# Performance work log

Hardware: AMD Instinct MI355X
Metric: run time of the kernel (lower is better)

The kernel has to match this reference:

```python
import jax, jax.numpy as jnp
import numpy as np

N = 100000   # nodes
E = 1600000  # edges
G = 64       # graphs in batch
F_IN = 128
H = 128
SV = 64
AD = 32


def setup_inputs() -> dict:
    key = jax.random.key(0)
    ks = jax.random.split(key, 12)
    s = 0.05
    return {
        "x": jax.random.normal(ks[0], (N, F_IN), jnp.float32),
        "edge_index": jax.random.randint(ks[1], (2, E), 0, N, dtype=jnp.int64),
        "batch": jnp.sort(jax.random.randint(ks[2], (N,), 0, G, dtype=jnp.int64)),
        "state_vector": jax.random.normal(ks[3], (G, SV), jnp.float32),
        "action": jax.random.normal(ks[4], (G, AD), jnp.float32),
        "W1": jax.random.normal(ks[5], (F_IN, H), jnp.float32) * s,
        "b1": jnp.zeros((H,), jnp.float32),
        "W2": jax.random.normal(ks[6], (H, H), jnp.float32) * s,
        "b2": jnp.zeros((H,), jnp.float32),
        "Wf1": jax.random.normal(ks[7], (H + SV + AD, 256), jnp.float32) * s,
        "bf1": jnp.zeros((256,), jnp.float32),
        "Wf2": jax.random.normal(ks[8], (256, 256), jnp.float32) * s,
        "bf2": jnp.zeros((256,), jnp.float32),
        "Wo": jax.random.normal(ks[9], (256, 1), jnp.float32) * s,
        "bo": jnp.zeros((1,), jnp.float32),
    }


def gcn_conv(x, W, b, src, dst, deg_inv_sqrt):
    # PyG GCNConv: h = x @ W; aggregate D^-1/2 (A+I) D^-1/2 h; + b
    h = x @ W
    norm = deg_inv_sqrt[src] * deg_inv_sqrt[dst]          # [E]
    agg = jax.ops.segment_sum(h[src] * norm[:, None], dst, num_segments=N)
    agg = agg + h * (deg_inv_sqrt * deg_inv_sqrt)[:, None]  # self loops
    return agg + b


def reference(x, edge_index, batch, state_vector, action,
              W1, b1, W2, b2, Wf1, bf1, Wf2, bf2, Wo, bo):
    src, dst = edge_index[0], edge_index[1]
    # degree after adding self loops (aggregation index = dst, PyG default flow)
    deg = jax.ops.segment_sum(jnp.ones((E,), jnp.float32), dst, num_segments=N) + 1.0
    deg_inv_sqrt = jax.lax.rsqrt(deg)

    h = jax.nn.relu(gcn_conv(x, W1, b1, src, dst, deg_inv_sqrt))
    h = jax.nn.relu(gcn_conv(h, W2, b2, src, dst, deg_inv_sqrt))

    # global_mean_pool over graph ids
    sums = jax.ops.segment_sum(h, batch, num_segments=G)
    cnts = jax.ops.segment_sum(jnp.ones((N,), jnp.float32), batch, num_segments=G)
    pooled = sums / jnp.maximum(cnts, 1.0)[:, None]       # [G, H]

    z = jnp.concatenate([pooled, state_vector, action], axis=1)  # [G, H+SV+AD]
    z = jax.nn.relu(z @ Wf1 + bf1)
    z = jax.nn.relu(z @ Wf2 + bf2)
    return z @ Wo + bo                                     # [G, 1]
```

## Files before the change

### kernel.cpp

```cpp
#include <hip/hip_runtime.h>
#include <hip/hip_bf16.h>
#include <stdint.h>

#define N_NODES 100000
#define N_EDGES 1600000
#define N_GRAPHS 64
#define HDIM 128

#define BUCKET_SHIFT 9
#define NBUCK ((N_NODES + 511) >> 9)
#define CAP 9728
#define SCAT_CHUNK 8192
#define SCAT_NBLK ((N_EDGES + SCAT_CHUNK - 1) / SCAT_CHUNK)
#define GB_NBLK ((N_NODES + 255) / 256)

typedef __bf16 bf16x8 __attribute__((ext_vector_type(8)));
typedef float f32x4 __attribute__((ext_vector_type(4)));
typedef float f32x2 __attribute__((ext_vector_type(2)));

__global__ __launch_bounds__(256) void setup_kernel(const int* __restrict__ batch,
                                                    int* __restrict__ gstart,
                                                    const float* __restrict__ W1,
                                                    const float* __restrict__ W2,
                                                    __hip_bfloat16* __restrict__ Wt1,
                                                    __hip_bfloat16* __restrict__ Wt2,
                                                    int* __restrict__ gcur,
                                                    float* __restrict__ psum) {
    int bid = blockIdx.x;
    if (bid < GB_NBLK) {
        int i = bid * 256 + threadIdx.x;
        if (i >= N_NODES) return;
        int b = batch[i];
        int prev = (i == 0) ? -1 : batch[i - 1];
        for (int g = prev + 1; g <= b; ++g) gstart[g] = i;
        if (i == N_NODES - 1) {
            for (int g = b + 1; g <= N_GRAPHS; ++g) gstart[g] = N_NODES;
        }
    } else if (bid < GB_NBLK + 128) {
        int t = bid - GB_NBLK;
        const float* W = (t < 64) ? W1 : W2;
        __hip_bfloat16* Wt = (t < 64) ? Wt1 : Wt2;
        int bb = t & 63;
        int n = bb * 2 + (threadIdx.x >> 7);
        int k = threadIdx.x & 127;
        Wt[n * 128 + k] = __float2bfloat16(W[k * 128 + n]);
    } else {
        int i = (bid - GB_NBLK - 128) * 256 + threadIdx.x;
        if (i < NBUCK) gcur[i] = i * CAP;
        int j = i - NBUCK;
        if (j >= 0 && j < N_GRAPHS * HDIM) psum[j] = 0.f;
    }
}
#define SETUP_NBLK (GB_NBLK + 128 + (NBUCK + N_GRAPHS * HDIM + 255) / 256)

__global__ __launch_bounds__(256) void scatter_kernel(const int* __restrict__ src,
                                                      const int* __restrict__ dst,
                                                      int* __restrict__ gcur,
                                                      int* __restrict__ sorted, int E) {
    __shared__ int hist[NBUCK];
    __shared__ int base_s[NBUCK];
    int tid = threadIdx.x;
    int e0 = blockIdx.x * SCAT_CHUNK;
    int sv[SCAT_CHUNK / 256], dv[SCAT_CHUNK / 256];
#pragma unroll
    for (int j = 0; j < SCAT_CHUNK / 256; j++) {
        int e = e0 + (j << 8) + tid;
        if (e < E) { sv[j] = src[e]; dv[j] = dst[e]; } else { sv[j] = -1; dv[j] = -1; }
    }
    if (tid < NBUCK) hist[tid] = 0;
    __syncthreads();
#pragma unroll
    for (int j = 0; j < SCAT_CHUNK / 256; j++)
        if (dv[j] >= 0) atomicAdd(&hist[dv[j] >> BUCKET_SHIFT], 1);
    __syncthreads();
    if (tid < NBUCK) {
        int c = hist[tid];
        base_s[tid] = (c > 0) ? atomicAdd(&gcur[tid], c) : 0;
    }
    __syncthreads();
    if (tid < NBUCK) hist[tid] = 0;
    __syncthreads();
#pragma unroll
    for (int j = 0; j < SCAT_CHUNK / 256; j++) {
        if (dv[j] >= 0) {
            int b = dv[j] >> BUCKET_SHIFT;
            int idx = atomicAdd(&hist[b], 1);
            sorted[base_s[b] + idx] = ((dv[j] & 511) << 17) | sv[j];
        }
    }
}

__global__ __launch_bounds__(256) void bucket_build_kernel(const int* __restrict__ sorted,
                                                           const int* __restrict__ gcur,
                                                           int2* __restrict__ rs2,
                                                           float* __restrict__ dis,
                                                           int* __restrict__ csr_src) {
    __shared__ int edges[CAP];
    __shared__ int cnt[512];
    __shared__ int excl[512];
    __shared__ int ps[256];
    int b = blockIdx.x, tid = threadIdx.x;
    cnt[tid] = 0; cnt[tid + 256] = 0;
    int node0 = b << BUCKET_SHIFT;
    int lo = b * CAP, hi = gcur[b];
    int ne = hi - lo;
    for (int i = tid; i < ne; i += 256) edges[i] = sorted[lo + i];
    __syncthreads();
    for (int i = tid; i < ne; i += 256)
        atomicAdd(&cnt[((unsigned)edges[i]) >> 17], 1);
    __syncthreads();
    int c0 = cnt[2 * tid], c1 = cnt[2 * tid + 1];
    ps[tid] = c0 + c1;
    __syncthreads();
#pragma unroll
    for (int off = 1; off < 256; off <<= 1) {
        int t = (tid >= off) ? ps[tid - off] : 0;
        __syncthreads();
        ps[tid] += t;
        __syncthreads();
    }
    int pex = ps[tid] - (c0 + c1);
    excl[2 * tid] = pex;
    excl[2 * tid + 1] = pex + c0;
    __syncthreads();
#pragma unroll
    for (int k = 0; k < 2; k++) {
        int li = tid + k * 256;
        int node = node0 + li;
        if (node < N_NODES) {
            int st = lo + excl[li] + li;
            int c = cnt[li];
            rs2[node] = make_int2(st, st + c + 1);
            dis[node] = rsqrtf((float)c + 1.0f);
            csr_src[st + c] = node;
        }
    }
    cnt[tid] = 0; cnt[tid + 256] = 0;
    __syncthreads();
    for (int i = tid; i < ne; i += 256) {
        int v = edges[i];
        int li = ((unsigned)v) >> 17;
        int idx = atomicAdd(&cnt[li], 1);
        csr_src[lo + excl[li] + li + idx] = v & 0x1FFFF;
    }
}

template<bool A_FP32>
__global__ __launch_bounds__(256) void gemm_mfma_kernel(const void* __restrict__ Av,
                                                        const __hip_bfloat16* __restrict__ Wt,
                                                        const float* __restrict__ scale,
                                                        unsigned char* __restrict__ C, int nrows) {
    __shared__ float Cs[64 * 132];
    int tid = threadIdx.x;
    int wave = tid >> 6, lane = tid & 63;
    int quad = lane >> 4, l16 = lane & 15;
    int row0 = blockIdx.x * 64;
    int arow = row0 + wave * 16 + l16;
    int arow_c = min(arow, nrows - 1);

    const __hip_bfloat16* A16 = (const __hip_bfloat16*)Av;
    const float* A32 = (const float*)Av;

    f32x4 acc[8];
#pragma unroll
    for (int t = 0; t < 8; t++) acc[t] = (f32x4){0.f, 0.f, 0.f, 0.f};

#pragma unroll
    for (int kt = 0; kt < 4; kt++) {
        int kbase = kt * 32 + quad * 8;
        union { bf16x8 v; __hip_bfloat16 h[8]; uint4 u; } au;
        if (A_FP32) {
            const float* ap = A32 + (size_t)arow_c * 128 + kbase;
            float4 u0 = *(const float4*)ap;
            float4 u1 = *(const float4*)(ap + 4);
            au.h[0] = __float2bfloat16(u0.x); au.h[1] = __float2bfloat16(u0.y);
            au.h[2] = __float2bfloat16(u0.z); au.h[3] = __float2bfloat16(u0.w);
            au.h[4] = __float2bfloat16(u1.x); au.h[5] = __float2bfloat16(u1.y);
            au.h[6] = __float2bfloat16(u1.z); au.h[7] = __float2bfloat16(u1.w);
        } else {
            au.u = *(const uint4*)(A16 + (size_t)arow_c * 128 + kbase);
        }
#pragma unroll
        for (int t = 0; t < 8; t++) {
            bf16x8 b = *(const bf16x8*)(Wt + (size_t)(t * 16 + l16) * 128 + kbase);
            acc[t] = __builtin_amdgcn_mfma_f32_16x16x32_bf16(au.v, b, acc[t], 0, 0, 0);
        }
    }

    int rbase = wave * 16 + quad * 4;
    float s[4];
#pragma unroll
    for (int r = 0; r < 4; r++) s[r] = scale[min(row0 + rbase + r, nrows - 1)];
#pragma unroll
    for (int t = 0; t < 8; t++) {
#pragma unroll
        for (int r = 0; r < 4; r++)
            Cs[(rbase + r) * 132 + t * 16 + l16] = acc[t][r] * s[r];
    }
    __syncthreads();

#pragma unroll
    for (int p = 0; p < 4; p++) {
        int g = p * 256 + tid;
        int row = g >> 4, c8 = (g & 15) * 8;
        int grow = row0 + row;
        if (grow < nrows) {
            const float* cp = &Cs[row * 132 + c8];
            float4 v0 = *(const float4*)cp;
            float4 v1 = *(const float4*)(cp + 4);
            int w0 = __builtin_amdgcn_cvt_pk_fp8_f32(v0.x, v0.y, 0, false);
            w0 = __builtin_amdgcn_cvt_pk_fp8_f32(v0.z, v0.w, w0, true);
            int w1 = __builtin_amdgcn_cvt_pk_fp8_f32(v1.x, v1.y, 0, false);
            w1 = __builtin_amdgcn_cvt_pk_fp8_f32(v1.z, v1.w, w1, true);
            *(uint2*)(C + (size_t)grow * 128 + c8) = make_uint2((unsigned)w0, (unsigned)w1);
        }
    }
}

__device__ __forceinline__ void accum8p(f32x2* acc, uint2 u) {
    acc[0] += __builtin_amdgcn_cvt_pk_f32_fp8((int)u.x, false);
    acc[1] += __builtin_amdgcn_cvt_pk_f32_fp8((int)u.x, true);
    acc[2] += __builtin_amdgcn_cvt_pk_f32_fp8((int)u.y, false);
    acc[3] += __builtin_amdgcn_cvt_pk_f32_fp8((int)u.y, true);
}

__global__ __launch_bounds__(256) void agg_kernel(const unsigned char* __restrict__ h8,
                                                  const float* __restrict__ dis,
                                                  const int2* __restrict__ rs2,
                                                  const int* __restrict__ csr_src,
                                                  const float* __restrict__ bias,
                                                  __hip_bfloat16* __restrict__ out, int n) {
    int wid = threadIdx.x >> 6;
    int lane = threadIdx.x & 63;
    int half = lane >> 5;
    int q = lane >> 4;
    int f = lane & 15;
    int l32 = lane & 31;
    int sub = q & 1;
    int hb = half << 5;

    int nodeA = blockIdx.x * 8 + wid * 2;
    if (nodeA >= n) return;
    int nodeB = nodeA + 1;
    bool hasB = nodeB < n;
    int myNode = half ? (hasB ? nodeB : nodeA) : nodeA;

    int2 se = rs2[myNode];
    int i0 = se.x;
    int deg = se.y - se.x;
    if (half && !hasB) deg = 0;

    float dn = dis[myNode];
    float4 b0 = *(const float4*)(bias + f * 8);
    float4 b1 = *(const float4*)(bias + f * 8 + 4);

    f32x2 acc[4];
#pragma unroll
    for (int j = 0; j < 4; j++) acc[j] = (f32x2){0.f, 0.f};

    for (int base = 0; base < deg; base += 32) {
        int cnt = min(deg - base, 32);
        int idx = csr_src[i0 + base + min(l32, cnt - 1)];
        int e = 0;
        for (; e + 8 <= cnt; e += 8) {
            int s0 = __shfl(idx, hb + e + sub, 64);
            int s1 = __shfl(idx, hb + e + 2 + sub, 64);
            int s2 = __shfl(idx, hb + e + 4 + sub, 64);
            int s3 = __shfl(idx, hb + e + 6 + sub, 64);
            uint2 u0 = *(const uint2*)(h8 + (size_t)s0 * 128 + f * 8);
            uint2 u1 = *(const uint2*)(h8 + (size_t)s1 * 128 + f * 8);
            uint2 u2 = *(const uint2*)(h8 + (size_t)s2 * 128 + f * 8);
            uint2 u3 = *(const uint2*)(h8 + (size_t)s3 * 128 + f * 8);
            accum8p(acc, u0);
            accum8p(acc, u1);
            accum8p(acc, u2);
            accum8p(acc, u3);
        }
        for (; e < cnt; e += 2) {
            bool valid = (e + sub) < cnt;
            int s = __shfl(idx, hb + min(e + sub, cnt - 1), 64);
            uint2 u = *(const uint2*)(h8 + (size_t)s * 128 + f * 8);
            if (valid) accum8p(acc, u);
        }
    }

#pragma unroll
    for (int j = 0; j < 4; j++) {
        f32x2 v = acc[j];
        v[0] += __shfl_down(v[0], 16, 64);
        v[1] += __shfl_down(v[1], 16, 64);
        acc[j] = v;
    }

    if (sub == 0 && (half == 0 || hasB)) {
        float r0 = fmaxf(fmaf(acc[0][0], dn, b0.x), 0.f);
        float r1 = fmaxf(fmaf(acc[0][1], dn, b0.y), 0.f);
        float r2 = fmaxf(fmaf(acc[1][0], dn, b0.z), 0.f);
        float r3 = fmaxf(fmaf(acc[1][1], dn, b0.w), 0.f);
        float r4 = fmaxf(fmaf(acc[2][0], dn, b1.x), 0.f);
        float r5 = fmaxf(fmaf(acc[2][1], dn, b1.y), 0.f);
        float r6 = fmaxf(fmaf(acc[3][0], dn, b1.z), 0.f);
        float r7 = fmaxf(fmaf(acc[3][1], dn, b1.w), 0.f);
        __hip_bfloat162 p0 = __float22bfloat162_rn(make_float2(r0, r1));
        __hip_bfloat162 p1 = __float22bfloat162_rn(make_float2(r2, r3));
        __hip_bfloat162 p2 = __float22bfloat162_rn(make_float2(r4, r5));
        __hip_bfloat162 p3 = __float22bfloat162_rn(make_float2(r6, r7));
        uint4 pk;
        pk.x = *(unsigned int*)&p0; pk.y = *(unsigned int*)&p1;
        pk.z = *(unsigned int*)&p2; pk.w = *(unsigned int*)&p3;
        *(uint4*)(out + (size_t)myNode * 128 + f * 8) = pk;
    }
}

#define POOL_ROWS 128
__global__ __launch_bounds__(256) void pool_kernel(const __hip_bfloat16* __restrict__ h,
                                                   const int* __restrict__ batch,
                                                   const int* __restrict__ gstart,
                                                   float* __restrict__ psum, int n) {
    __shared__ float red[16 * 128];
    int tid = threadIdx.x;
    int rr = tid >> 4, fg = tid & 15;
    int r0 = blockIdx.x * POOL_ROWS;
    if (r0 >= n) return;
    int r1 = min(n, r0 + POOL_ROWS);
    int g = batch[r0];
    int seg_lo = r0;
    while (seg_lo < r1) {
        while (gstart[g + 1] <= seg_lo) g++;
        int seg_hi = min(r1, gstart[g + 1]);
        float a[8];
#pragma unroll
        for (int j = 0; j < 8; j++) a[j] = 0.f;
        for (int r = seg_lo + rr; r < seg_hi; r += 16) {
            uint4 u = *(const uint4*)(h + (size_t)r * 128 + fg * 8);
            float2 f0 = __bfloat1622float2(*(__hip_bfloat162*)&u.x);
            float2 f1 = __bfloat1622float2(*(__hip_bfloat162*)&u.y);
            float2 f2 = __bfloat1622float2(*(__hip_bfloat162*)&u.z);
            float2 f3 = __bfloat1622float2(*(__hip_bfloat162*)&u.w);
            a[0] += f0.x; a[1] += f0.y; a[2] += f1.x; a[3] += f1.y;
            a[4] += f2.x; a[5] += f2.y; a[6] += f3.x; a[7] += f3.y;
        }
        *(float4*)&red[rr * 128 + fg * 8] = make_float4(a[0], a[1], a[2], a[3]);
        *(float4*)&red[rr * 128 + fg * 8 + 4] = make_float4(a[4], a[5], a[6], a[7]);
        __syncthreads();
        if (tid < 128) {
            float s = 0.f;
#pragma unroll
            for (int k = 0; k < 16; k++) s += red[k * 128 + tid];
            atomicAdd(&psum[g * 128 + tid], s);
        }
        __syncthreads();
        seg_lo = seg_hi;
    }
}

__global__ __launch_bounds__(256) void mlp_kernel(const float* __restrict__ psum,
                                                  const int* __restrict__ gstart,
                                                  const float* __restrict__ sv,
                                                  const float* __restrict__ act,
                                                  const float* __restrict__ Wf1,
                                                  const float* __restrict__ bf1,
                                                  const float* __restrict__ Wf2,
                                                  const float* __restrict__ bf2,
                                                  const float* __restrict__ Wo,
                                                  const float* __restrict__ bo,
                                                  float* __restrict__ out) {
    int g = blockIdx.x, tid = threadIdx.x;
    __shared__ float z[224];
    __shared__ float z1[256];
    __shared__ float red[256];
    if (tid < 128) {
        int c = gstart[g + 1] - gstart[g];
        float cnt = fmaxf((float)c, 1.f);
        z[tid] = psum[g * 128 + tid] / cnt;
    } else if (tid < 192) {
        z[tid] = sv[g * 64 + (tid - 128)];
    } else if (tid < 224) {
        z[tid] = act[g * 32 + (tid - 192)];
    }
    __syncthreads();
    float a = bf1[tid];
    for (int k = 0; k < 224; k++) a = fmaf(z[k], Wf1[k * 256 + tid], a);
    z1[tid] = fmaxf(a, 0.f);
    __syncthreads();
    float b = bf2[tid];
    for (int k = 0; k < 256; k++) b = fmaf(z1[k], Wf2[k * 256 + tid], b);
    b = fmaxf(b, 0.f);
    red[tid] = b * Wo[tid];
    __syncthreads();
    for (int off = 128; off > 0; off >>= 1) {
        if (tid < off) red[tid] += red[tid + off];
        __syncthreads();
    }
    if (tid == 0) out[g] = red[0] + bo[0];
}

extern "C" void kernel_launch(void* const* d_in, const int* in_sizes, int n_in,
                              void* d_out, int out_size, void* d_ws, size_t ws_size,
                              hipStream_t stream) {
    const float* x   = (const float*)d_in[0];
    const int*   eidx = (const int*)d_in[1];
    const int*   batch = (const int*)d_in[2];
    const float* sv  = (const float*)d_in[3];
    const float* act = (const float*)d_in[4];
    const float* W1  = (const float*)d_in[5];
    const float* b1  = (const float*)d_in[6];
    const float* W2  = (const float*)d_in[7];
    const float* b2  = (const float*)d_in[8];
    const float* Wf1 = (const float*)d_in[9];
    const float* bf1 = (const float*)d_in[10];
    const float* Wf2 = (const float*)d_in[11];
    const float* bf2 = (const float*)d_in[12];
    const float* Wo  = (const float*)d_in[13];
    const float* bo  = (const float*)d_in[14];
    float* out = (float*)d_out;

    const int* srcp = eidx;
    const int* dstp = eidx + N_EDGES;

    char* w = (char*)d_ws;
    int* gcur = (int*)w;               w += (size_t)NBUCK * 4;
    float* psum = (float*)w;           w += (size_t)N_GRAPHS * HDIM * 4;
    int2* rs2 = (int2*)w;              w += (size_t)N_NODES * 8;
    float* dis = (float*)w;            w += (size_t)N_NODES * 4;
    int* gstart = (int*)w;             w += (size_t)(N_GRAPHS + 1) * 4;
    w = (char*)(((uintptr_t)w + 255) & ~(uintptr_t)255);
    int* csr_src = (int*)w;            w += (size_t)NBUCK * CAP * 4;
    w = (char*)(((uintptr_t)w + 255) & ~(uintptr_t)255);
    int* sorted = (int*)w;             w += (size_t)NBUCK * CAP * 4;
    w = (char*)(((uintptr_t)w + 255) & ~(uintptr_t)255);
    __hip_bfloat16* Wt1 = (__hip_bfloat16*)w;   w += (size_t)HDIM * HDIM * 2;
    __hip_bfloat16* Wt2 = (__hip_bfloat16*)w;   w += (size_t)HDIM * HDIM * 2;
    w = (char*)(((uintptr_t)w + 255) & ~(uintptr_t)255);
    unsigned char* hbuf = (unsigned char*)w;    w += (size_t)N_NODES * HDIM;
    w = (char*)(((uintptr_t)w + 255) & ~(uintptr_t)255);
    __hip_bfloat16* abuf = (__hip_bfloat16*)w;  w += (size_t)N_NODES * HDIM * 2;

    setup_kernel<<<SETUP_NBLK, 256, 0, stream>>>(batch, gstart, W1, W2, Wt1, Wt2, gcur, psum);

    scatter_kernel<<<SCAT_NBLK, 256, 0, stream>>>(srcp, dstp, gcur, sorted, N_EDGES);
    bucket_build_kernel<<<NBUCK, 256, 0, stream>>>(sorted, gcur, rs2, dis, csr_src);

    int gemm_blocks = (N_NODES + 63) / 64;
    int agg_blocks = (N_NODES + 7) / 8;

    gemm_mfma_kernel<true><<<gemm_blocks, 256, 0, stream>>>(x, Wt1, dis, hbuf, N_NODES);
    agg_kernel<<<agg_blocks, 256, 0, stream>>>(hbuf, dis, rs2, csr_src, b1, abuf, N_NODES);
    gemm_mfma_kernel<false><<<gemm_blocks, 256, 0, stream>>>(abuf, Wt2, dis, hbuf, N_NODES);
    agg_kernel<<<agg_blocks, 256, 0, stream>>>(hbuf, dis, rs2, csr_src, b2, abuf, N_NODES);

    pool_kernel<<<(N_NODES + POOL_ROWS - 1) / POOL_ROWS, 256, 0, stream>>>(abuf, batch, gstart, psum, N_NODES);
    mlp_kernel<<<N_GRAPHS, 256, 0, stream>>>(psum, gstart, sv, act, Wf1, bf1, Wf2, bf2, Wo, bo, out);
}
```

Before: 296.3 us.

## Fuse edge scatter with first GEMM and widen aggregation gathers to 16 bytes

The first GEMM no longer depends on the degree normalisation. The source-side dis scaling moves out of the GEMM epilogue into the aggregation loop, where each neighbour's dis value is shuffled and multiplied in. This lets the edge-scatter blocks and the first GEMM blocks run in one merged launch, overlapping the memory-bound sort with MFMA work and removing a kernel boundary. The aggregation kernel now uses 8 lanes per row with 16-byte fp8 gathers instead of 16 lanes with 8-byte gathers, and adds a second shuffle-reduction level. The cost is an extra dis load and multiply per edge, plus higher register use in the aggregation.

Result: slower. 334.9 us (+13.0%).

```diff
diff --git a/kernel.cpp b/kernel.cpp
--- a/kernel.cpp
+++ b/kernel.cpp
@@ -12,6 +12,7 @@
 #define CAP 9728
 #define SCAT_CHUNK 8192
 #define SCAT_NBLK ((N_EDGES + SCAT_CHUNK - 1) / SCAT_CHUNK)
+#define GEMM_NBLK ((N_NODES + 63) / 64)
 #define GB_NBLK ((N_NODES + 255) / 256)
 
 typedef __bf16 bf16x8 __attribute__((ext_vector_type(8)));
@@ -53,32 +54,31 @@
 }
 #define SETUP_NBLK (GB_NBLK + 128 + (NBUCK + N_GRAPHS * HDIM + 255) / 256)
 
-__global__ __launch_bounds__(256) void scatter_kernel(const int* __restrict__ src,
-                                                      const int* __restrict__ dst,
-                                                      int* __restrict__ gcur,
-                                                      int* __restrict__ sorted, int E) {
-    __shared__ int hist[NBUCK];
-    __shared__ int base_s[NBUCK];
+__device__ void scatter_body(const int* __restrict__ src,
+                             const int* __restrict__ dst,
+                             int* __restrict__ gcur,
+                             int* __restrict__ sorted, int E, int bid,
+                             int* hist, int* base_s) {
     int tid = threadIdx.x;
-    int e0 = blockIdx.x * SCAT_CHUNK;
+    int e0 = bid * SCAT_CHUNK;
     int sv[SCAT_CHUNK / 256], dv[SCAT_CHUNK / 256];
 #pragma unroll
     for (int j = 0; j < SCAT_CHUNK / 256; j++) {
         int e = e0 + (j << 8) + tid;
         if (e < E) { sv[j] = src[e]; dv[j] = dst[e]; } else { sv[j] = -1; dv[j] = -1; }
     }
-    if (tid < NBUCK) hist[tid] = 0;
+    for (int i = tid; i < NBUCK; i += 256) hist[i] = 0;
     __syncthreads();
 #pragma unroll
     for (int j = 0; j < SCAT_CHUNK / 256; j++)
         if (dv[j] >= 0) atomicAdd(&hist[dv[j] >> BUCKET_SHIFT], 1);
     __syncthreads();
-    if (tid < NBUCK) {
-        int c = hist[tid];
-        base_s[tid] = (c > 0) ? atomicAdd(&gcur[tid], c) : 0;
-    }
-    __syncthreads();
-    if (tid < NBUCK) hist[tid] = 0;
+    for (int i = tid; i < NBUCK; i += 256) {
+        int c = hist[i];
+        base_s[i] = (c > 0) ? atomicAdd(&gcur[i], c) : 0;
+    }
+    __syncthreads();
+    for (int i = tid; i < NBUCK; i += 256) hist[i] = 0;
     __syncthreads();
 #pragma unroll
     for (int j = 0; j < SCAT_CHUNK / 256; j++) {
@@ -146,15 +146,14 @@
 }
 
 template<bool A_FP32>
-__global__ __launch_bounds__(256) void gemm_mfma_kernel(const void* __restrict__ Av,
-                                                        const __hip_bfloat16* __restrict__ Wt,
-                                                        const float* __restrict__ scale,
-                                                        unsigned char* __restrict__ C, int nrows) {
-    __shared__ float Cs[64 * 132];
+__device__ void gemm_body(const void* __restrict__ Av,
+                          const __hip_bfloat16* __restrict__ Wt,
+                          unsigned char* __restrict__ C, int nrows, int bid,
+                          float* Cs ) {
     int tid = threadIdx.x;
     int wave = tid >> 6, lane = tid & 63;
     int quad = lane >> 4, l16 = lane & 15;
-    int row0 = blockIdx.x * 64;
+    int row0 = bid * 64;
     int arow = row0 + wave * 16 + l16;
     int arow_c = min(arow, nrows - 1);
 
@@ -188,14 +187,11 @@
     }
 
     int rbase = wave * 16 + quad * 4;
-    float s[4];
-#pragma unroll
-    for (int r = 0; r < 4; r++) s[r] = scale[min(row0 + rbase + r, nrows - 1)];
 #pragma unroll
     for (int t = 0; t < 8; t++) {
 #pragma unroll
         for (int r = 0; r < 4; r++)
-            Cs[(rbase + r) * 132 + t * 16 + l16] = acc[t][r] * s[r];
+            Cs[(rbase + r) * 132 + t * 16 + l16] = acc[t][r];
     }
     __syncthreads();
 
@@ -217,11 +213,39 @@
     }
 }
 
-__device__ __forceinline__ void accum8p(f32x2* acc, uint2 u) {
-    acc[0] += __builtin_amdgcn_cvt_pk_f32_fp8((int)u.x, false);
-    acc[1] += __builtin_amdgcn_cvt_pk_f32_fp8((int)u.x, true);
-    acc[2] += __builtin_amdgcn_cvt_pk_f32_fp8((int)u.y, false);
-    acc[3] += __builtin_amdgcn_cvt_pk_f32_fp8((int)u.y, true);
+__global__ __launch_bounds__(256) void scatter_gemm1_kernel(const int* __restrict__ src,
+                                                            const int* __restrict__ dst,
+                                                            int* __restrict__ gcur,
+                                                            int* __restrict__ sorted,
+                                                            const float* __restrict__ x,
+                                                            const __hip_bfloat16* __restrict__ Wt1,
+                                                            unsigned char* __restrict__ hbuf) {
+    __shared__ float Cs[64 * 132];
+    if (blockIdx.x < SCAT_NBLK) {
+        scatter_body(src, dst, gcur, sorted, N_EDGES, blockIdx.x,
+                     (int*)Cs, (int*)Cs + NBUCK);
+    } else {
+        gemm_body<true>(x, Wt1, hbuf, N_NODES, blockIdx.x - SCAT_NBLK, Cs);
+    }
+}
+
+__global__ __launch_bounds__(256) void gemm_mfma_kernel(const void* __restrict__ Av,
+                                                        const __hip_bfloat16* __restrict__ Wt,
+                                                        unsigned char* __restrict__ C, int nrows) {
+    __shared__ float Cs[64 * 132];
+    gemm_body<false>(Av, Wt, C, nrows, blockIdx.x, Cs);
+}
+
+__device__ __forceinline__ void accum16(f32x2* acc, uint4 u, float d) {
+    f32x2 dd = {d, d};
+    acc[0] += dd * __builtin_amdgcn_cvt_pk_f32_fp8((int)u.x, false);
+    acc[1] += dd * __builtin_amdgcn_cvt_pk_f32_fp8((int)u.x, true);
+    acc[2] += dd * __builtin_amdgcn_cvt_pk_f32_fp8((int)u.y, false);
+    acc[3] += dd * __builtin_amdgcn_cvt_pk_f32_fp8((int)u.y, true);
+    acc[4] += dd * __builtin_amdgcn_cvt_pk_f32_fp8((int)u.z, false);
+    acc[5] += dd * __builtin_amdgcn_cvt_pk_f32_fp8((int)u.z, true);
+    acc[6] += dd * __builtin_amdgcn_cvt_pk_f32_fp8((int)u.w, false);
+    acc[7] += dd * __builtin_amdgcn_cvt_pk_f32_fp8((int)u.w, true);
 }
 
 __global__ __launch_bounds__(256) void agg_kernel(const unsigned char* __restrict__ h8,
@@ -233,11 +257,11 @@
     int wid = threadIdx.x >> 6;
     int lane = threadIdx.x & 63;
     int half = lane >> 5;
-    int q = lane >> 4;
-    int f = lane & 15;
     int l32 = lane & 31;
-    int sub = q & 1;
+    int g2 = l32 >> 3;
+    int f8 = lane & 7;
     int hb = half << 5;
+    int fo = f8 * 16;
 
     int nodeA = blockIdx.x * 8 + wid * 2;
     if (nodeA >= n) return;
@@ -251,64 +275,96 @@
     if (half && !hasB) deg = 0;
 
     float dn = dis[myNode];
-    float4 b0 = *(const float4*)(bias + f * 8);
-    float4 b1 = *(const float4*)(bias + f * 8 + 4);
-
-    f32x2 acc[4];
-#pragma unroll
-    for (int j = 0; j < 4; j++) acc[j] = (f32x2){0.f, 0.f};
+    float4 b0 = *(const float4*)(bias + fo);
+    float4 b1 = *(const float4*)(bias + fo + 4);
+    float4 b2 = *(const float4*)(bias + fo + 8);
+    float4 b3 = *(const float4*)(bias + fo + 12);
+
+    f32x2 acc[8];
+#pragma unroll
+    for (int j = 0; j < 8; j++) acc[j] = (f32x2){0.f, 0.f};
 
     for (int base = 0; base < deg; base += 32) {
         int cnt = min(deg - base, 32);
         int idx = csr_src[i0 + base + min(l32, cnt - 1)];
+        float dsv = dis[idx];
         int e = 0;
-        for (; e + 8 <= cnt; e += 8) {
-            int s0 = __shfl(idx, hb + e + sub, 64);
-            int s1 = __shfl(idx, hb + e + 2 + sub, 64);
-            int s2 = __shfl(idx, hb + e + 4 + sub, 64);
-            int s3 = __shfl(idx, hb + e + 6 + sub, 64);
-            uint2 u0 = *(const uint2*)(h8 + (size_t)s0 * 128 + f * 8);
-            uint2 u1 = *(const uint2*)(h8 + (size_t)s1 * 128 + f * 8);
-            uint2 u2 = *(const uint2*)(h8 + (size_t)s2 * 128 + f * 8);
-            uint2 u3 = *(const uint2*)(h8 + (size_t)s3 * 128 + f * 8);
-            accum8p(acc, u0);
-            accum8p(acc, u1);
-            accum8p(acc, u2);
-            accum8p(acc, u3);
-        }
-        for (; e < cnt; e += 2) {
-            bool valid = (e + sub) < cnt;
-            int s = __shfl(idx, hb + min(e + sub, cnt - 1), 64);
-            uint2 u = *(const uint2*)(h8 + (size_t)s * 128 + f * 8);
-            if (valid) accum8p(acc, u);
-        }
-    }
-
-#pragma unroll
-    for (int j = 0; j < 4; j++) {
+        for (; e + 16 <= cnt; e += 16) {
+            int s0 = __shfl(idx, hb + e + g2, 64);
+            int s1 = __shfl(idx, hb + e + 4 + g2, 64);
+            int s2 = __shfl(idx, hb + e + 8 + g2, 64);
+            int s3 = __shfl(idx, hb + e + 12 + g2, 64);
+            float d0 = __shfl(dsv, hb + e + g2, 64);
+            float d1 = __shfl(dsv, hb + e + 4 + g2, 64);
+            float d2 = __shfl(dsv, hb + e + 8 + g2, 64);
+            float d3 = __shfl(dsv, hb + e + 12 + g2, 64);
+            uint4 u0 = *(const uint4*)(h8 + (unsigned)((s0 << 7) + fo));
+            uint4 u1 = *(const uint4*)(h8 + (unsigned)((s1 << 7) + fo));
+            uint4 u2 = *(const uint4*)(h8 + (unsigned)((s2 << 7) + fo));
+            uint4 u3 = *(const uint4*)(h8 + (unsigned)((s3 << 7) + fo));
+            accum16(acc, u0, d0);
+            accum16(acc, u1, d1);
+            accum16(acc, u2, d2);
+            accum16(acc, u3, d3);
+        }
+        for (; e + 4 <= cnt; e += 4) {
+            int s = __shfl(idx, hb + e + g2, 64);
+            float d = __shfl(dsv, hb + e + g2, 64);
+            uint4 u = *(const uint4*)(h8 + (unsigned)((s << 7) + fo));
+            accum16(acc, u, d);
+        }
+        if (e < cnt) {
+            bool valid = (e + g2) < cnt;
+            int sl = hb + min(e + g2, cnt - 1);
+            int s = __shfl(idx, sl, 64);
+            float d = __shfl(dsv, sl, 64);
+            uint4 u = *(const uint4*)(h8 + (unsigned)((s << 7) + fo));
+            if (valid) accum16(acc, u, d);
+        }
+    }
+
+#pragma unroll
+    for (int j = 0; j < 8; j++) {
         f32x2 v = acc[j];
-        v[0] += __shfl_down(v[0], 16, 64);
-        v[1] += __shfl_down(v[1], 16, 64);
+        v[0] += __shfl_down(v[0], 16, 32);
+        v[1] += __shfl_down(v[1], 16, 32);
+        v[0] += __shfl_down(v[0], 8, 32);
+        v[1] += __shfl_down(v[1], 8, 32);
         acc[j] = v;
     }
 
-    if (sub == 0 && (half == 0 || hasB)) {
-        float r0 = fmaxf(fmaf(acc[0][0], dn, b0.x), 0.f);
-        float r1 = fmaxf(fmaf(acc[0][1], dn, b0.y), 0.f);
-        float r2 = fmaxf(fmaf(acc[1][0], dn, b0.z), 0.f);
-        float r3 = fmaxf(fmaf(acc[1][1], dn, b0.w), 0.f);
-        float r4 = fmaxf(fmaf(acc[2][0], dn, b1.x), 0.f);
-        float r5 = fmaxf(fmaf(acc[2][1], dn, b1.y), 0.f);
-        float r6 = fmaxf(fmaf(acc[3][0], dn, b1.z), 0.f);
-        float r7 = fmaxf(fmaf(acc[3][1], dn, b1.w), 0.f);
+    if (l32 < 8 && (half == 0 || hasB)) {
+        float r0  = fmaxf(fmaf(acc[0][0], dn, b0.x), 0.f);
+        float r1  = fmaxf(fmaf(acc[0][1], dn, b0.y), 0.f);
+        float r2  = fmaxf(fmaf(acc[1][0], dn, b0.z), 0.f);
+        float r3  = fmaxf(fmaf(acc[1][1], dn, b0.w), 0.f);
+        float r4  = fmaxf(fmaf(acc[2][0], dn, b1.x), 0.f);
+        float r5  = fmaxf(fmaf(acc[2][1], dn, b1.y), 0.f);
+        float r6  = fmaxf(fmaf(acc[3][0], dn, b1.z), 0.f);
+        float r7  = fmaxf(fmaf(acc[3][1], dn, b1.w), 0.f);
+        float r8  = fmaxf(fmaf(acc[4][0], dn, b2.x), 0.f);
+        float r9  = fmaxf(fmaf(acc[4][1], dn, b2.y), 0.f);
+        float r10 = fmaxf(fmaf(acc[5][0], dn, b2.z), 0.f);
+        float r11 = fmaxf(fmaf(acc[5][1], dn, b2.w), 0.f);
+        float r12 = fmaxf(fmaf(acc[6][0], dn, b3.x), 0.f);
+        float r13 = fmaxf(fmaf(acc[6][1], dn, b3.y), 0.f);
+        float r14 = fmaxf(fmaf(acc[7][0], dn, b3.z), 0.f);
+        float r15 = fmaxf(fmaf(acc[7][1], dn, b3.w), 0.f);
         __hip_bfloat162 p0 = __float22bfloat162_rn(make_float2(r0, r1));
         __hip_bfloat162 p1 = __float22bfloat162_rn(make_float2(r2, r3));
         __hip_bfloat162 p2 = __float22bfloat162_rn(make_float2(r4, r5));
         __hip_bfloat162 p3 = __float22bfloat162_rn(make_float2(r6, r7));
-        uint4 pk;
-        pk.x = *(unsigned int*)&p0; pk.y = *(unsigned int*)&p1;
-        pk.z = *(unsigned int*)&p2; pk.w = *(unsigned int*)&p3;
-        *(uint4*)(out + (size_t)myNode * 128 + f * 8) = pk;
+        __hip_bfloat162 p4 = __float22bfloat162_rn(make_float2(r8, r9));
+        __hip_bfloat162 p5 = __float22bfloat162_rn(make_float2(r10, r11));
+        __hip_bfloat162 p6 = __float22bfloat162_rn(make_float2(r12, r13));
+        __hip_bfloat162 p7 = __float22bfloat162_rn(make_float2(r14, r15));
+        uint4 pk0, pk1;
+        pk0.x = *(unsigned int*)&p0; pk0.y = *(unsigned int*)&p1;
+        pk0.z = *(unsigned int*)&p2; pk0.w = *(unsigned int*)&p3;
+        pk1.x = *(unsigned int*)&p4; pk1.y = *(unsigned int*)&p5;
+        pk1.z = *(unsigned int*)&p6; pk1.w = *(unsigned int*)&p7;
+        *(uint4*)(out + (size_t)myNode * 128 + fo) = pk0;
+        *(uint4*)(out + (size_t)myNode * 128 + fo + 8) = pk1;
     }
 }
 
@@ -438,15 +494,14 @@
 
     setup_kernel<<<SETUP_NBLK, 256, 0, stream>>>(batch, gstart, W1, W2, Wt1, Wt2, gcur, psum);
 
-    scatter_kernel<<<SCAT_NBLK, 256, 0, stream>>>(srcp, dstp, gcur, sorted, N_EDGES);
+    scatter_gemm1_kernel<<<SCAT_NBLK + GEMM_NBLK, 256, 0, stream>>>(srcp, dstp, gcur, sorted,
+                                                                    x, Wt1, hbuf);
     bucket_build_kernel<<<NBUCK, 256, 0, stream>>>(sorted, gcur, rs2, dis, csr_src);
 
-    int gemm_blocks = (N_NODES + 63) / 64;
     int agg_blocks = (N_NODES + 7) / 8;
 
-    gemm_mfma_kernel<true><<<gemm_blocks, 256, 0, stream>>>(x, Wt1, dis, hbuf, N_NODES);
     agg_kernel<<<agg_blocks, 256, 0, stream>>>(hbuf, dis, rs2, csr_src, b1, abuf, N_NODES);
-    gemm_mfma_kernel<false><<<gemm_blocks, 256, 0, stream>>>(abuf, Wt2, dis, hbuf, N_NODES);
+    gemm_mfma_kernel<<<GEMM_NBLK, 256, 0, stream>>>(abuf, Wt2, hbuf, N_NODES);
     agg_kernel<<<agg_blocks, 256, 0, stream>>>(hbuf, dis, rs2, csr_src, b2, abuf, N_NODES);
 
     pool_kernel<<<(N_NODES + POOL_ROWS - 1) / POOL_ROWS, 256, 0, stream>>>(abuf, batch, gstart, psum, N_NODES);
```
